# Kernel optimization log

Hardware: AMD Instinct MI355X
Metric: run time of the kernel (lower is better)

The kernel has to match this reference:

```python
import jax, jax.numpy as jnp
import numpy as np

H = 512      # hidden_size
E = 256      # encoding_size
L = 64       # latent_dim
O = 2        # output_size
NH = 4       # num_heads
HD = H // NH # head dim
BS = 1024
S = 100      # encoded source length
T = 30       # decode steps


def setup_inputs() -> dict:
    key = jax.random.key(0)
    ks = jax.random.split(key, 26)
    def p(k, shape, s=0.05):
        return jax.random.normal(k, shape, dtype=jnp.float32) * s
    return {
        "encoded": jax.random.normal(ks[0], (BS, S, E), dtype=jnp.float32),
        "z": jax.random.normal(ks[1], (BS, T, L), dtype=jnp.float32),
        # MultiheadAttention params (separate q/k/v projections since kdim!=embed_dim)
        "q_w": p(ks[2], (H, H)), "k_w": p(ks[3], (H, E)), "v_w": p(ks[4], (H, E)),
        "q_b": p(ks[5], (H,)), "k_b": p(ks[6], (H,)), "v_b": p(ks[7], (H,)),
        "out_w": p(ks[8], (H, H)), "out_b": p(ks[9], (H,)),
        # fc_layer1: Linear(H+L, H)
        "fc1_w": p(ks[10], (H, H + L)), "fc1_b": p(ks[11], (H,)),
        # LSTMCell 1 and 2 (gate order i,f,g,o)
        "l1_wih": p(ks[12], (4 * H, H)), "l1_whh": p(ks[13], (4 * H, H)),
        "l1_bih": p(ks[14], (4 * H,)), "l1_bhh": p(ks[15], (4 * H,)),
        "l2_wih": p(ks[16], (4 * H, H)), "l2_whh": p(ks[17], (4 * H, H)),
        "l2_bih": p(ks[18], (4 * H,)), "l2_bhh": p(ks[19], (4 * H,)),
        # fc_layer2: H -> H/2 -> H/4 -> O
        "fc2a_w": p(ks[20], (H // 2, H)), "fc2a_b": p(ks[21], (H // 2,)),
        "fc2b_w": p(ks[22], (H // 4, H // 2)), "fc2b_b": p(ks[23], (H // 4,)),
        "fc2c_w": p(ks[24], (O, H // 4)), "fc2c_b": p(ks[25], (O,)),
    }


def _lrelu(x):
    return jnp.where(x >= 0, x, 0.2 * x)


def _lstm_cell(x, h, c, wih, whh, bih, bhh):
    g = x @ wih.T + bih + h @ whh.T + bhh
    i, f, gg, o = jnp.split(g, 4, axis=-1)
    c2 = jax.nn.sigmoid(f) * c + jax.nn.sigmoid(i) * jnp.tanh(gg)
    h2 = jax.nn.sigmoid(o) * jnp.tanh(c2)
    return h2, c2


def _forward(encoded, z, q_w, k_w, v_w, q_b, k_b, v_b, out_w, out_b,
             fc1_w, fc1_b, l1_wih, l1_whh, l1_bih, l1_bhh,
             l2_wih, l2_whh, l2_bih, l2_bhh,
             fc2a_w, fc2a_b, fc2b_w, fc2b_b, fc2c_w, fc2c_b):
    bs, s, _ = encoded.shape
    # K/V projections depend only on encoded -> compute once: [bs, NH, S, HD]
    k = (encoded @ k_w.T + k_b).reshape(bs, s, NH, HD).transpose(0, 2, 1, 3)
    v = (encoded @ v_w.T + v_b).reshape(bs, s, NH, HD).transpose(0, 2, 1, 3)
    scale = 1.0 / jnp.sqrt(jnp.float32(HD))

    def step(carry, zt):
        att_in, h1, c1, h2, c2 = carry  # all [bs, H]
        # single-query attention (query len 1); dropout inactive in eval
        q = ((att_in @ q_w.T + q_b) * scale).reshape(bs, NH, HD)
        attw = jax.nn.softmax(jnp.einsum('bnd,bnsd->bns', q, k), axis=-1)
        att = jnp.einsum('bns,bnsd->bnd', attw, v).reshape(bs, H)
        att = att @ out_w.T + out_b
        out = _lrelu(jnp.concatenate([att, zt], axis=-1) @ fc1_w.T + fc1_b)
        h1, c1 = _lstm_cell(out, h1, c1, l1_wih, l1_whh, l1_bih, l1_bhh)
        h2, c2 = _lstm_cell(h1, h2, c2, l2_wih, l2_whh, l2_bih, l2_bhh)
        y = _lrelu(h2 @ fc2a_w.T + fc2a_b)
        y = _lrelu(y @ fc2b_w.T + fc2b_b)
        y = jnp.tanh(y @ fc2c_w.T + fc2c_b)  # [bs, O]
        return (h2, h1, c1, h2, c2), y

    zer = jnp.zeros((bs, H), dtype=encoded.dtype)
    init = (zer, zer, zer, zer, zer)
    _, ys = jax.lax.scan(step, init, jnp.swapaxes(z, 0, 1))  # ys: [T, bs, O]
    return jnp.swapaxes(ys, 0, 1)  # [bs, T, O]


def reference(encoded, z, q_w, k_w, v_w, q_b, k_b, v_b, out_w, out_b,
              fc1_w, fc1_b, l1_wih, l1_whh, l1_bih, l1_bhh,
              l2_wih, l2_whh, l2_bih, l2_bhh,
              fc2a_w, fc2a_b, fc2b_w, fc2b_b, fc2c_w, fc2c_b):
    return _forward(encoded, z, q_w, k_w, v_w, q_b, k_b, v_b, out_w, out_b,
                    fc1_w, fc1_b, l1_wih, l1_whh, l1_bih, l1_bhh,
                    l2_wih, l2_whh, l2_bih, l2_bhh,
                    fc2a_w, fc2a_b, fc2b_w, fc2b_b, fc2c_w, fc2c_b)
```

## Files before the change

kernel.cpp:

```cpp
#include <hip/hip_runtime.h>


#define DEVI __device__ __forceinline__

typedef _Float16 f16x8 __attribute__((ext_vector_type(8)));
typedef _Float16 f16x4 __attribute__((ext_vector_type(4)));
typedef float    f32x4 __attribute__((ext_vector_type(4)));
typedef unsigned u32x4 __attribute__((ext_vector_type(4)));
typedef unsigned u32x2 __attribute__((ext_vector_type(2)));

#define BSZ 1024
#define SEQ 100
#define ENC 256
#define HID 512
#define LAT 64
#define TT  30

DEVI float lrelu(float v) { return v >= 0.f ? v : 0.2f * v; }
DEVI float sigm(float x)  { return 1.f / (1.f + __expf(-x)); }
DEVI float tanh_f(float x){ return 1.f - 2.f / (1.f + __expf(2.f * x)); }

DEVI void wait_vm0() { asm volatile("s_waitcnt vmcnt(0)" ::: "memory"); }
DEVI u32x4 ld_sc_b128(const void* p) {
    u32x4 d;
    asm volatile("global_load_dwordx4 %0, %1, off sc0 sc1" : "=v"(d) : "v"(p) : "memory");
    return d;
}
DEVI void st_sc_b128(void* p, u32x4 v) {
    asm volatile("global_store_dwordx4 %0, %1, off sc0 sc1" :: "v"(p), "v"(v) : "memory");
}
DEVI void st_sc_b64(void* p, u32x2 v) {
    asm volatile("global_store_dwordx2 %0, %1, off sc0 sc1" :: "v"(p), "v"(v) : "memory");
}

__global__ __launch_bounds__(256) void zero_ws(uint4* __restrict__ p) {
    uint4 z; z.x = z.y = z.z = z.w = 0u;
    p[(size_t)blockIdx.x * 256 + threadIdx.x] = z;
}

__global__ __launch_bounds__(256) void conv_enc(const float4* __restrict__ src,
                                                f16x4* __restrict__ dst) {
    size_t i = (size_t)blockIdx.x * 256 + threadIdx.x;
    float4 v = src[i];
    f16x4 h;
    h.x = (_Float16)v.x; h.y = (_Float16)v.y; h.z = (_Float16)v.z; h.w = (_Float16)v.w;
    dst[i] = h;
}

__global__ __launch_bounds__(256) void prep_qk(const float* __restrict__ k_w,
                                               const float* __restrict__ q_w,
                                               const float* __restrict__ q_b,
                                               _Float16* __restrict__ C_h,
                                               float* __restrict__ d_f,
                                               _Float16* __restrict__ d_h) {
    const int ne = blockIdx.x, n = ne >> 8, e = ne & 255, tid = threadIdx.x;
    const float scale = 0.08838834764831845f;
    float a0 = 0.f, a1 = 0.f;
    for (int dd = 0; dd < 128; ++dd) {
        float kv = k_w[(n * 128 + dd) * 256 + e];
        a0 += kv * q_w[(n * 128 + dd) * 512 + tid];
        a1 += kv * q_w[(n * 128 + dd) * 512 + 256 + tid];
    }
    C_h[(size_t)ne * 512 + tid]       = (_Float16)(scale * a0);
    C_h[(size_t)ne * 512 + 256 + tid] = (_Float16)(scale * a1);
    float pq = (tid < 128) ? k_w[(n * 128 + tid) * 256 + e] * q_b[n * 128 + tid] : 0.f;
    #pragma unroll
    for (int off = 32; off; off >>= 1) pq += __shfl_down(pq, off);
    __shared__ float red[4];
    if ((tid & 63) == 0) red[tid >> 6] = pq;
    __syncthreads();
    if (tid == 0) {
        float s = scale * (red[0] + red[1] + red[2] + red[3]);
        d_f[ne] = s; d_h[ne] = (_Float16)s;
    }
}

__global__ __launch_bounds__(256) void prep_A(const float* __restrict__ fc1_w,
                                              const float* __restrict__ out_w,
                                              float* __restrict__ A) {
    const int h = blockIdx.x, tid = threadIdx.x;
    float a0 = 0.f, a1 = 0.f;
    for (int m = 0; m < 512; ++m) {
        float fv = fc1_w[h * 576 + m];
        a0 += fv * out_w[m * 512 + tid];
        a1 += fv * out_w[m * 512 + 256 + tid];
    }
    A[(size_t)h * 512 + tid]       = a0;
    A[(size_t)h * 512 + 256 + tid] = a1;
}

__global__ __launch_bounds__(256) void prep_wfc1(const float* __restrict__ A,
                                                 const float* __restrict__ v_w,
                                                 const float* __restrict__ v_b,
                                                 const float* __restrict__ fc1_w,
                                                 const float* __restrict__ out_b,
                                                 const float* __restrict__ fc1_b,
                                                 _Float16* __restrict__ Wfc1,
                                                 float* __restrict__ biasf) {
    const int h = blockIdx.x, tid = threadIdx.x;
    #pragma unroll
    for (int g = 0; g < 4; ++g) {
        float acc = 0.f;
        for (int dd = 0; dd < 128; ++dd)
            acc += A[h * 512 + g * 128 + dd] * v_w[(g * 128 + dd) * 256 + tid];
        Wfc1[(size_t)h * 1088 + g * 256 + tid] = (_Float16)acc;
    }
    if (tid < 64)
        Wfc1[(size_t)h * 1088 + 1024 + tid] = (_Float16)fc1_w[h * 576 + 512 + tid];
    float ps = A[h * 512 + tid] * v_b[tid] + A[h * 512 + 256 + tid] * v_b[256 + tid]
             + fc1_w[h * 576 + tid] * out_b[tid] + fc1_w[h * 576 + 256 + tid] * out_b[256 + tid];
    #pragma unroll
    for (int off = 32; off; off >>= 1) ps += __shfl_down(ps, off);
    __shared__ float red[4];
    if ((tid & 63) == 0) red[tid >> 6] = ps;
    __syncthreads();
    if (tid == 0) biasf[h] = red[0] + red[1] + red[2] + red[3] + fc1_b[h];
}

__global__ __launch_bounds__(256) void prep_lstm(const float* __restrict__ wih,
                                                 const float* __restrict__ whh,
                                                 const float* __restrict__ bih,
                                                 const float* __restrict__ bhh,
                                                 _Float16* __restrict__ Wc,
                                                 float* __restrict__ bc) {
    int idx = blockIdx.x * 256 + threadIdx.x;
    int rp = idx >> 10, cc = idx & 1023;
    int h = rp >> 2, g = rp & 3;
    int rsrc = g * 512 + h;
    float v = (cc < 512) ? wih[(size_t)rsrc * 512 + cc] : whh[(size_t)rsrc * 512 + cc - 512];
    Wc[idx] = (_Float16)v;
    if (idx < 2048) {
        int h2 = idx >> 2, g2 = idx & 3;
        bc[idx] = bih[g2 * 512 + h2] + bhh[g2 * 512 + h2];
    }
}

__global__ __launch_bounds__(256) void prep_fc2c(const float* __restrict__ aw,
                                                 const float* __restrict__ bw,
                                                 const float* __restrict__ cw,
                                                 _Float16* __restrict__ a16,
                                                 _Float16* __restrict__ b16,
                                                 _Float16* __restrict__ c16) {
    int i = blockIdx.x * 256 + threadIdx.x;
    if (i < 131072) a16[i] = (_Float16)aw[i];
    else if (i < 163840) b16[i - 131072] = (_Float16)bw[i - 131072];
    else if (i < 164096) c16[i - 163840] = (_Float16)cw[i - 163840];
}

template <int NTHR, int BM, int BN, int BK, int WM, int WN, bool BYPX>
DEVI void gemm_core_db(char* smem_raw, const _Float16* __restrict__ X, int ldx,
                       const _Float16* __restrict__ W, int ldw, int K,
                       int bm0, int bn0, f32x4* acc) {
    constexpr int LDT = BK + 8;
    _Float16* Xs = (_Float16*)smem_raw;
    _Float16* Ws = Xs + BM * LDT;
    const int tid = threadIdx.x, wave = tid >> 6, lane = tid & 63;
    constexpr int WROWS = BM / WM;
    static_assert(WROWS * (BN / WN) == NTHR / 64, "wave grid mismatch");
    const int wm = wave % WROWS, wn = wave / WROWS;
    constexpr int MT = WM / 16, NT = WN / 16;
    const int q = lane >> 4, m15 = lane & 15;
    constexpr int CPR = BK / 8;
    constexpr int XCH = BM * CPR, WCH = BN * CPR;
    constexpr int XPT = (XCH + NTHR - 1) / NTHR;
    constexpr int WPT = (WCH + NTHR - 1) / NTHR;
    u32x4 xr[XPT], wr[WPT];
    auto ldregs = [&](int k0) {
        #pragma unroll
        for (int c = 0; c < XPT; ++c) {
            int cc = tid + c * NTHR;
            if ((XCH % NTHR) == 0 || cc < XCH) {
                int row = cc / CPR, col = (cc % CPR) * 8;
                const void* px = &X[(size_t)(bm0 + row) * ldx + k0 + col];
                if (BYPX) xr[c] = ld_sc_b128(px);
                else      xr[c] = *(const u32x4*)px;
            }
        }
        #pragma unroll
        for (int c = 0; c < WPT; ++c) {
            int cc = tid + c * NTHR;
            if ((WCH % NTHR) == 0 || cc < WCH) {
                int row = cc / CPR, col = (cc % CPR) * 8;
                wr[c] = *(const u32x4*)&W[(size_t)(bn0 + row) * ldw + k0 + col];
            }
        }
    };
    ldregs(0);
    for (int k0 = 0; k0 < K; k0 += BK) {
        if (BYPX) wait_vm0();
        #pragma unroll
        for (int c = 0; c < XPT; ++c) {
            int cc = tid + c * NTHR;
            if ((XCH % NTHR) == 0 || cc < XCH) {
                int row = cc / CPR, col = (cc % CPR) * 8;
                *(u32x4*)&Xs[row * LDT + col] = xr[c];
            }
        }
        #pragma unroll
        for (int c = 0; c < WPT; ++c) {
            int cc = tid + c * NTHR;
            if ((WCH % NTHR) == 0 || cc < WCH) {
                int row = cc / CPR, col = (cc % CPR) * 8;
                *(u32x4*)&Ws[row * LDT + col] = wr[c];
            }
        }
        __syncthreads();
        if (k0 + BK < K) ldregs(k0 + BK);
        #pragma unroll
        for (int kk = 0; kk < BK / 32; ++kk) {
            f16x8 af[MT], bf[NT];
            #pragma unroll
            for (int i = 0; i < MT; ++i)
                af[i] = *(const f16x8*)&Xs[(wm * WM + i * 16 + m15) * LDT + kk * 32 + q * 8];
            #pragma unroll
            for (int j = 0; j < NT; ++j)
                bf[j] = *(const f16x8*)&Ws[(wn * WN + j * 16 + m15) * LDT + kk * 32 + q * 8];
            #pragma unroll
            for (int i = 0; i < MT; ++i)
                #pragma unroll
                for (int j = 0; j < NT; ++j)
                    acc[i * NT + j] = __builtin_amdgcn_mfma_f32_16x16x32_f16(af[i], bf[j], acc[i * NT + j], 0, 0, 0);
        }
        __syncthreads();
    }
}

template <int NTHR, int BM, int BN, int WM, int WN, int ACT>
DEVI void epi_staged(char* smem_raw, const f32x4* acc, const float* __restrict__ bias,
                     _Float16* __restrict__ out, int ldo, int bm0, int bn0) {
    constexpr int LDS_ = BN + 4;
    float* accs = (float*)smem_raw;
    const int tid = threadIdx.x, wave = tid >> 6, lane = tid & 63;
    constexpr int WROWS = BM / WM;
    const int wm = wave % WROWS, wn = wave / WROWS;
    constexpr int MT = WM / 16, NT = WN / 16;
    const int q = lane >> 4, m15 = lane & 15;
    #pragma unroll
    for (int i = 0; i < MT; ++i) {
        #pragma unroll
        for (int j = 0; j < NT; ++j) {
            int cl = wn * WN + j * 16 + m15;
            float bv = bias[bn0 + cl];
            #pragma unroll
            for (int r = 0; r < 4; ++r) {
                int rl = wm * WM + i * 16 + q * 4 + r;
                float v = acc[i * NT + j][r] + bv;
                if (ACT == 1) v = lrelu(v);
                accs[rl * LDS_ + cl] = v;
            }
        }
    }
    __syncthreads();
    constexpr int CH = BN / 8, ITEMS = BM * CH;
    #pragma unroll
    for (int base = 0; base < ITEMS; base += NTHR) {
        int idx = base + tid;
        if ((ITEMS % NTHR) == 0 || idx < ITEMS) {
            int row = idx / CH, ch = idx % CH;
            const float* src = &accs[row * LDS_ + ch * 8];
            f16x8 o;
            #pragma unroll
            for (int k = 0; k < 8; ++k) o[k] = (_Float16)src[k];
            st_sc_b128(&out[(size_t)(bm0 + row) * ldo + bn0 + ch * 8],
                       __builtin_bit_cast(u32x4, o));
        }
    }
    __syncthreads();
}

DEVI void gbar(unsigned* bars, int grp, unsigned want) {
    wait_vm0();
    __syncthreads();
    if (threadIdx.x == 0) {
        unsigned* cnt  = &bars[grp * 64];
        unsigned* flag = &bars[grp * 64 + 32];
        unsigned a = __hip_atomic_fetch_add(cnt, 1u, __ATOMIC_RELEASE, __HIP_MEMORY_SCOPE_AGENT);
        if (a == 15u) {
            __hip_atomic_store(cnt, 0u, __ATOMIC_RELAXED, __HIP_MEMORY_SCOPE_AGENT);
            __hip_atomic_store(flag, want, __ATOMIC_RELEASE, __HIP_MEMORY_SCOPE_AGENT);
        }
        unsigned spins = 0;
        while (__hip_atomic_load(flag, __ATOMIC_RELAXED, __HIP_MEMORY_SCOPE_AGENT) < want) {
            __builtin_amdgcn_s_sleep(1);
            if (++spins > (1u << 16)) break;
        }
        asm volatile("" ::: "memory");
    }
    __syncthreads();
}

DEVI void attn_phase(char* smem, const _Float16* __restrict__ G,
                     const _Float16* __restrict__ encH, const float* __restrict__ z,
                     _Float16* __restrict__ eb, int b0, int t) {
    _Float16* encs = (_Float16*)smem;
    _Float16* gs   = (_Float16*)(smem + 51200);
    float* sc      = (float*)(smem + 59392);
    float* wsm     = (float*)(smem + 61440);
    f32x4* part    = (f32x4*)(smem + 63488);
    const int tid = threadIdx.x;
    u32x4 r[7];
    auto ldenc = [&](int b) {
        const u32x4* src = (const u32x4*)(encH + (size_t)b * (SEQ * ENC));
        #pragma unroll
        for (int i = 0; i < 6; ++i) r[i] = src[tid + i * 512];
        if (tid < 128) r[6] = src[tid + 3072];
    };
    ldenc(b0);
    u32x4 gv;
    {
        int row = tid >> 7, idx = tid & 127;
        gv = ld_sc_b128(&G[(size_t)(b0 + row) * 1024 + idx * 8]);
    }
    wait_vm0();
    {
        int row = tid >> 7, idx = tid & 127;
        *(u32x4*)&gs[row * 1024 + idx * 8] = gv;
    }
    for (int i = 0; i < 4; ++i) {
        {
            u32x4* dst = (u32x4*)encs;
            #pragma unroll
            for (int k = 0; k < 6; ++k) dst[tid + k * 512] = r[k];
            if (tid < 128) dst[tid + 3072] = r[6];
        }
        __syncthreads();
        if (i < 3) ldenc(b0 + i + 1);
        const int b = b0 + i;
        {
            const int grpq = tid >> 4, l16 = tid & 15, n = grpq & 3, soff = grpq >> 2;
            const f16x8 g0 = *(const f16x8*)&gs[i * 1024 + n * 256 + l16 * 8];
            const f16x8 g1 = *(const f16x8*)&gs[i * 1024 + n * 256 + 128 + l16 * 8];
            for (int it = 0; it < 13; ++it) {
                int s = it * 8 + soff;
                if (s < SEQ) {
                    const f16x8 e0 = *(const f16x8*)&encs[s * ENC + l16 * 8];
                    const f16x8 e1 = *(const f16x8*)&encs[s * ENC + 128 + l16 * 8];
                    float p = 0.f;
                    #pragma unroll
                    for (int j = 0; j < 8; ++j)
                        p += (float)e0[j] * (float)g0[j] + (float)e1[j] * (float)g1[j];
                    p += __shfl_xor(p, 1); p += __shfl_xor(p, 2);
                    p += __shfl_xor(p, 4); p += __shfl_xor(p, 8);
                    if (l16 == 0) sc[n * 128 + s] = p;
                }
            }
        }
        __syncthreads();
        const int wv = tid >> 6, ln = tid & 63;
        if (wv < 4) {
            float v0 = sc[wv * 128 + ln];
            float v1 = (ln < SEQ - 64) ? sc[wv * 128 + 64 + ln] : -1e30f;
            float m = fmaxf(v0, v1);
            #pragma unroll
            for (int off = 32; off; off >>= 1) m = fmaxf(m, __shfl_xor(m, off));
            float e0 = __expf(v0 - m);
            float e1 = (ln < SEQ - 64) ? __expf(v1 - m) : 0.f;
            float ss = e0 + e1;
            #pragma unroll
            for (int off = 32; off; off >>= 1) ss += __shfl_xor(ss, off);
            float inv = 1.f / ss;
            wsm[wv * 128 + ln] = e0 * inv;
            if (ln < SEQ - 64) wsm[wv * 128 + 64 + ln] = e1 * inv;
        }
        __syncthreads();
        {
            const int n = wv & 3, half = wv >> 2;
            float a0 = 0.f, a1 = 0.f, a2 = 0.f, a3 = 0.f;
            const int sBeg = half * 50, sEnd = sBeg + 50;
            #pragma unroll 5
            for (int s = sBeg; s < sEnd; ++s) {
                f16x4 e4 = *(const f16x4*)&encs[s * ENC + ln * 4];
                float w = wsm[n * 128 + s];
                a0 += w * (float)e4.x; a1 += w * (float)e4.y;
                a2 += w * (float)e4.z; a3 += w * (float)e4.w;
            }
            f32x4 pv; pv[0] = a0; pv[1] = a1; pv[2] = a2; pv[3] = a3;
            part[wv * 64 + ln] = pv;
        }
        __syncthreads();
        if (tid < 128) {
            int n = tid >> 5, t8 = tid & 31;
            f32x4 a  = part[n * 64 + t8 * 2];
            f32x4 b2 = part[n * 64 + t8 * 2 + 1];
            f32x4 c  = part[(n + 4) * 64 + t8 * 2];
            f32x4 d  = part[(n + 4) * 64 + t8 * 2 + 1];
            f16x8 o;
            o[0] = (_Float16)(a[0] + c[0]); o[1] = (_Float16)(a[1] + c[1]);
            o[2] = (_Float16)(a[2] + c[2]); o[3] = (_Float16)(a[3] + c[3]);
            o[4] = (_Float16)(b2[0] + d[0]); o[5] = (_Float16)(b2[1] + d[1]);
            o[6] = (_Float16)(b2[2] + d[2]); o[7] = (_Float16)(b2[3] + d[3]);
            st_sc_b128(&eb[(size_t)b * 1088 + n * 256 + t8 * 8],
                       __builtin_bit_cast(u32x4, o));
        } else if (tid < 144) {
            int k = tid - 128;
            float4 zv = *(const float4*)&z[((size_t)b * TT + t) * 64 + k * 4];
            f16x4 zh;
            zh.x = (_Float16)zv.x; zh.y = (_Float16)zv.y;
            zh.z = (_Float16)zv.z; zh.w = (_Float16)zv.w;
            st_sc_b64(&eb[(size_t)b * 1088 + 1024 + k * 4],
                      __builtin_bit_cast(u32x2, zh));
        }
        __syncthreads();
    }
}

DEVI void lstm_phase(char* smem, const _Float16* __restrict__ X,
                     const _Float16* __restrict__ W, const float* __restrict__ bias,
                     float (&cr)[8], _Float16* __restrict__ hA, int ldA,
                     int bm0, int bn0) {
    f32x4 acc[4] = {};
    gemm_core_db<512, 64, 128, 128, 32, 32, true>(smem, X, 1024, W, 1024, 1024, bm0, bn0, acc);
    float* accs = (float*)smem;
    const int tid = threadIdx.x, wave = tid >> 6, lane = tid & 63;
    const int wm = wave & 1, wn = wave >> 1, q = lane >> 4, m15 = lane & 15;
    #pragma unroll
    for (int i = 0; i < 2; ++i) {
        #pragma unroll
        for (int j = 0; j < 2; ++j) {
            int cl = wn * 32 + j * 16 + m15;
            float bv = bias[bn0 + cl];
            #pragma unroll
            for (int r = 0; r < 4; ++r) {
                int rl = wm * 32 + i * 16 + q * 4 + r;
                accs[rl * 132 + cl] = acc[i * 2 + j][r] + bv;
            }
        }
    }
    __syncthreads();
    if (tid < 256) {
        int bl = tid >> 2, ch = tid & 3;
        const float4* gp = (const float4*)&accs[bl * 132 + ch * 32];
        f16x8 hv;
        #pragma unroll
        for (int j = 0; j < 8; ++j) {
            float4 g4 = gp[j];
            float cn = sigm(g4.y) * cr[j] + sigm(g4.x) * tanh_f(g4.z);
            cr[j] = cn;
            hv[j] = (_Float16)(sigm(g4.w) * tanh_f(cn));
        }
        int h0 = (bn0 >> 2) + ch * 8, gb = bm0 + bl;
        st_sc_b128(&hA[(size_t)gb * ldA + h0], __builtin_bit_cast(u32x4, hv));
    }
    __syncthreads();
}

DEVI void fc2_512(char* smem, const _Float16* __restrict__ h2n,
                  const _Float16* __restrict__ Wa, const float* __restrict__ ab,
                  const _Float16* __restrict__ Wb, const float* __restrict__ bb,
                  const _Float16* __restrict__ Wc, const float* __restrict__ cb,
                  float* __restrict__ out, int b0, int t) {
    _Float16* h2s = (_Float16*)smem;
    _Float16* y1s = h2s + 16 * 520;
    _Float16* y2s = y1s + 16 * 264;
    const int tid = threadIdx.x, wave = tid >> 6, lane = tid & 63;
    const int q = lane >> 4, m15 = lane & 15;
    u32x4 hv[2];
    #pragma unroll
    for (int c = 0; c < 2; ++c) {
        int cc = tid + c * 512, row = cc >> 6, col = (cc & 63) * 8;
        hv[c] = ld_sc_b128(&h2n[(size_t)(b0 + row) * 512 + col]);
    }
    wait_vm0();
    #pragma unroll
    for (int c = 0; c < 2; ++c) {
        int cc = tid + c * 512, row = cc >> 6, col = (cc & 63) * 8;
        *(u32x4*)&h2s[row * 520 + col] = hv[c];
    }
    __syncthreads();
    {
        f32x4 acc[2] = {};
        #pragma unroll 4
        for (int kk = 0; kk < 16; ++kk) {
            f16x8 af = *(const f16x8*)&h2s[m15 * 520 + kk * 32 + q * 8];
            #pragma unroll
            for (int j = 0; j < 2; ++j) {
                int n = wave * 32 + j * 16 + m15;
                f16x8 bf = *(const f16x8*)&Wa[(size_t)n * 512 + kk * 32 + q * 8];
                acc[j] = __builtin_amdgcn_mfma_f32_16x16x32_f16(af, bf, acc[j], 0, 0, 0);
            }
        }
        #pragma unroll
        for (int j = 0; j < 2; ++j) {
            int col = wave * 32 + j * 16 + m15;
            float bv = ab[col];
            #pragma unroll
            for (int r = 0; r < 4; ++r)
                y1s[(q * 4 + r) * 264 + col] = (_Float16)lrelu(acc[j][r] + bv);
        }
    }
    __syncthreads();
    {
        f32x4 acc[1] = {};
        #pragma unroll
        for (int kk = 0; kk < 8; ++kk) {
            f16x8 af = *(const f16x8*)&y1s[m15 * 264 + kk * 32 + q * 8];
            int n = wave * 16 + m15;
            f16x8 bf = *(const f16x8*)&Wb[(size_t)n * 256 + kk * 32 + q * 8];
            acc[0] = __builtin_amdgcn_mfma_f32_16x16x32_f16(af, bf, acc[0], 0, 0, 0);
        }
        int col = wave * 16 + m15;
        float bv = bb[col];
        #pragma unroll
        for (int r = 0; r < 4; ++r)
            y2s[(q * 4 + r) * 136 + col] = (_Float16)lrelu(acc[0][r] + bv);
    }
    __syncthreads();
    if (tid < 32) {
        int r = tid >> 1, o = tid & 1;
        float acc = cb[o];
        #pragma unroll 8
        for (int k = 0; k < 128; ++k)
            acc += (float)Wc[o * 128 + k] * (float)y2s[r * 136 + k];
        out[((size_t)(b0 + r) * TT + t) * 2 + o] = tanhf(acc);
    }
}

struct DecP {
    const _Float16* encH;
    const float* z;
    _Float16* eb;
    const _Float16* Wfc1;  const float* biasf;
    const _Float16* L1W;   const float* L1b;
    const _Float16* L2W;   const float* L2b;
    const _Float16* C_h;   const float* d_f;  const _Float16* d_h;
    const _Float16* fa;    const float* fab;
    const _Float16* fb;    const float* fbb;
    const _Float16* fcw;   const float* fcb;
    _Float16* xh1;  _Float16* xh2;  _Float16* h2n;  _Float16* G;
    float* out;
    unsigned* bars;
};

__global__ __launch_bounds__(512, 1) void decoder(DecP p) {
    __shared__ __align__(16) char smem[71680];
    const int blk = blockIdx.x, tid = threadIdx.x;
    const int grp = blk >> 4, sub = blk & 15;
    const int b0a = blk * 4;
    const int bm0 = grp * 64;
    float c1r[8] = {}, c2r[8] = {};
    unsigned want = 0;
    if (tid < 128) {
        u32x4 v = *(const u32x4*)&p.d_h[tid * 8];
        #pragma unroll
        for (int i = 0; i < 4; ++i)
            st_sc_b128(&p.G[(size_t)(b0a + i) * 1024 + tid * 8], v);
    }
    wait_vm0();
    __syncthreads();
    for (int t = 0; t < TT; ++t) {
        attn_phase(smem, p.G, p.encH, p.z, p.eb, b0a, t);
        gbar(p.bars, grp, ++want);
        {
            f32x4 acc[1] = {};
            gemm_core_db<512, 64, 32, 64, 16, 16, true>(smem, p.eb, 1088, p.Wfc1, 1088, 1088,
                                                        bm0, sub * 32, acc);
            epi_staged<512, 64, 32, 16, 16, 1>(smem, acc, p.biasf, p.xh1, 1024, bm0, sub * 32);
        }
        gbar(p.bars, grp, ++want);
        lstm_phase(smem, p.xh1, p.L1W, p.L1b, c1r, p.xh2, 1024, bm0, sub * 128);
        gbar(p.bars, grp, ++want);
        lstm_phase(smem, p.xh2, p.L2W, p.L2b, c2r, p.h2n, 512, bm0, sub * 128);
        gbar(p.bars, grp, ++want);
        if (t < TT - 1) {
            {
                int idx = tid & 255, row = idx >> 2, ch = idx & 3;
                size_t ro = (size_t)(bm0 + row);
                const void* src; void* dst;
                if (tid < 256) {
                    src = &p.xh2[ro * 1024 + sub * 32 + ch * 8];
                    dst = &p.xh1[ro * 1024 + 512 + sub * 32 + ch * 8];
                } else {
                    src = &p.h2n[ro * 512 + sub * 32 + ch * 8];
                    dst = &p.xh2[ro * 1024 + 512 + sub * 32 + ch * 8];
                }
                u32x4 v = ld_sc_b128(src);
                wait_vm0();
                st_sc_b128(dst, v);
            }
            f32x4 acc[2] = {};
            gemm_core_db<512, 64, 64, 128, 16, 32, true>(smem, p.h2n, 512, p.C_h, 512, 512,
                                                         bm0, sub * 64, acc);
            epi_staged<512, 64, 64, 16, 32, 0>(smem, acc, p.d_f, p.G, 1024, bm0, sub * 64);
        }
        if (sub < 4)
            fc2_512(smem, p.h2n, p.fa, p.fab, p.fb, p.fbb, p.fcw, p.fcb,
                    p.out, bm0 + sub * 16, t);
        if (t < TT - 1) gbar(p.bars, grp, ++want);
    }
}

extern "C" void kernel_launch(void* const* d_in, const int* in_sizes, int n_in,
                              void* d_out, int out_size, void* d_ws, size_t ws_size,
                              hipStream_t stream) {
    const float* encoded = (const float*)d_in[0];
    const float* z       = (const float*)d_in[1];
    const float* q_w     = (const float*)d_in[2];
    const float* k_w     = (const float*)d_in[3];
    const float* v_w     = (const float*)d_in[4];
    const float* q_b     = (const float*)d_in[5];
    const float* v_b     = (const float*)d_in[7];
    const float* out_w   = (const float*)d_in[8];
    const float* out_b   = (const float*)d_in[9];
    const float* fc1_w   = (const float*)d_in[10];
    const float* fc1_b   = (const float*)d_in[11];
    const float* l1_wih  = (const float*)d_in[12];
    const float* l1_whh  = (const float*)d_in[13];
    const float* l1_bih  = (const float*)d_in[14];
    const float* l1_bhh  = (const float*)d_in[15];
    const float* l2_wih  = (const float*)d_in[16];
    const float* l2_whh  = (const float*)d_in[17];
    const float* l2_bih  = (const float*)d_in[18];
    const float* l2_bhh  = (const float*)d_in[19];
    const float* fc2a_w  = (const float*)d_in[20];
    const float* fc2a_b  = (const float*)d_in[21];
    const float* fc2b_w  = (const float*)d_in[22];
    const float* fc2b_b  = (const float*)d_in[23];
    const float* fc2c_w  = (const float*)d_in[24];
    const float* fc2c_b  = (const float*)d_in[25];
    float* out = (float*)d_out;

    char* p = (char*)d_ws;
    auto take = [&](size_t bytes) { char* r = p; p += (bytes + 255) & ~(size_t)255; return r; };
    _Float16* encH  = (_Float16*)take(52428800);
    _Float16* C_h   = (_Float16*)take(1048576);
    _Float16* Wfc1  = (_Float16*)take(1114112);
    _Float16* L1W   = (_Float16*)take(4194304);
    _Float16* L2W   = (_Float16*)take(4194304);
    _Float16* fc2a16= (_Float16*)take(262144);
    _Float16* fc2b16= (_Float16*)take(65536);
    _Float16* fc2c16= (_Float16*)take(512);
    _Float16* eb    = (_Float16*)take(2228224);
    _Float16* h2n   = (_Float16*)take(1048576);
    char* zreg = p;
    _Float16* xh1 = (_Float16*)take(2097152);
    _Float16* xh2 = (_Float16*)take(2097152);
    unsigned* bars = (unsigned*)take(4096);
    _Float16* G   = (_Float16*)take(2097152);
    float* A      = (float*)take(1048576);
    float* d_f    = (float*)take(4096);
    _Float16* d_h = (_Float16*)take(2048);
    float* biasf  = (float*)take(2048);
    float* L1b    = (float*)take(8192);
    float* L2b    = (float*)take(8192);
    (void)in_sizes; (void)n_in; (void)out_size; (void)ws_size;

    zero_ws<<<1025, 256, 0, stream>>>((uint4*)zreg);
    conv_enc<<<25600, 256, 0, stream>>>((const float4*)encoded, (f16x4*)encH);
    prep_qk<<<1024, 256, 0, stream>>>(k_w, q_w, q_b, C_h, d_f, d_h);
    prep_A<<<512, 256, 0, stream>>>(fc1_w, out_w, A);
    prep_wfc1<<<512, 256, 0, stream>>>(A, v_w, v_b, fc1_w, out_b, fc1_b, Wfc1, biasf);
    prep_lstm<<<8192, 256, 0, stream>>>(l1_wih, l1_whh, l1_bih, l1_bhh, L1W, L1b);
    prep_lstm<<<8192, 256, 0, stream>>>(l2_wih, l2_whh, l2_bih, l2_bhh, L2W, L2b);
    prep_fc2c<<<641, 256, 0, stream>>>(fc2a_w, fc2b_w, fc2c_w, fc2a16, fc2b16, fc2c16);

    DecP dp;
    dp.encH = encH; dp.z = z; dp.eb = eb;
    dp.Wfc1 = Wfc1; dp.biasf = biasf;
    dp.L1W = L1W; dp.L1b = L1b; dp.L2W = L2W; dp.L2b = L2b;
    dp.C_h = C_h; dp.d_f = d_f; dp.d_h = d_h;
    dp.fa = fc2a16; dp.fab = fc2a_b; dp.fb = fc2b16; dp.fbb = fc2b_b;
    dp.fcw = fc2c16; dp.fcb = fc2c_b;
    dp.xh1 = xh1; dp.xh2 = xh2; dp.h2n = h2n; dp.G = G;
    dp.out = out; dp.bars = bars;
    void* params[] = { &dp };
    if (hipLaunchCooperativeKernel((const void*)decoder, dim3(256), dim3(512),
                                   params, 0, stream) != hipSuccess) {
        decoder<<<256, 512, 0, stream>>>(dp);
    }
}
```

Baseline: 3.309 ms.

## Keep encoder slices resident in LDS/registers, double-buffer hidden state, flag-array barrier

Each block now loads its four encoder slices once before the decode loop, one into shared memory and three into registers, instead of re-reading them from global memory on every step. The recurrent hidden-state buffers are double-buffered, and the LSTM epilogue writes h into the next step's input buffer directly, which removes the copy phase. The group barrier swaps the atomic counter for per-block flag stores that every block polls with vector loads. The cost is a much larger register footprint (84 extra u32x4 per thread) and more shared memory. Launch bounds also change to 2 blocks per CU, which could spill or hurt occupancy.

```diff
diff --git a/kernel.cpp b/kernel.cpp
--- a/kernel.cpp
+++ b/kernel.cpp
@@ -19,6 +19,7 @@
 DEVI float lrelu(float v) { return v >= 0.f ? v : 0.2f * v; }
 DEVI float sigm(float x)  { return 1.f / (1.f + __expf(-x)); }
 DEVI float tanh_f(float x){ return 1.f - 2.f / (1.f + __expf(2.f * x)); }
+DEVI unsigned umin2(unsigned a, unsigned b) { return a < b ? a : b; }
 
 DEVI void wait_vm0() { asm volatile("s_waitcnt vmcnt(0)" ::: "memory"); }
 DEVI u32x4 ld_sc_b128(const void* p) {
@@ -31,6 +32,9 @@
 }
 DEVI void st_sc_b64(void* p, u32x2 v) {
     asm volatile("global_store_dwordx2 %0, %1, off sc0 sc1" :: "v"(p), "v"(v) : "memory");
+}
+DEVI void st_sc_b32(void* p, unsigned v) {
+    asm volatile("global_store_dword %0, %1, off sc0 sc1" :: "v"(p), "v"(v) : "memory");
 }
 
 __global__ __launch_bounds__(256) void zero_ws(uint4* __restrict__ p) {
@@ -268,146 +272,148 @@
     __syncthreads();
 }
 
-DEVI void gbar(unsigned* bars, int grp, unsigned want) {
+DEVI void gbar(unsigned* bars, int grp, int sub, unsigned want) {
     wait_vm0();
     __syncthreads();
     if (threadIdx.x == 0) {
-        unsigned* cnt  = &bars[grp * 64];
-        unsigned* flag = &bars[grp * 64 + 32];
-        unsigned a = __hip_atomic_fetch_add(cnt, 1u, __ATOMIC_RELEASE, __HIP_MEMORY_SCOPE_AGENT);
-        if (a == 15u) {
-            __hip_atomic_store(cnt, 0u, __ATOMIC_RELAXED, __HIP_MEMORY_SCOPE_AGENT);
-            __hip_atomic_store(flag, want, __ATOMIC_RELEASE, __HIP_MEMORY_SCOPE_AGENT);
-        }
+        st_sc_b32(&bars[grp * 16 + sub], want);
         unsigned spins = 0;
-        while (__hip_atomic_load(flag, __ATOMIC_RELAXED, __HIP_MEMORY_SCOPE_AGENT) < want) {
+        for (;;) {
+            u32x4 a = ld_sc_b128(&bars[grp * 16 + 0]);
+            u32x4 b = ld_sc_b128(&bars[grp * 16 + 4]);
+            u32x4 c = ld_sc_b128(&bars[grp * 16 + 8]);
+            u32x4 d = ld_sc_b128(&bars[grp * 16 + 12]);
+            wait_vm0();
+            unsigned mn = umin2(umin2(umin2(a[0], a[1]), umin2(a[2], a[3])),
+                          umin2(umin2(umin2(b[0], b[1]), umin2(b[2], b[3])),
+                          umin2(umin2(umin2(c[0], c[1]), umin2(c[2], c[3])),
+                                umin2(umin2(d[0], d[1]), umin2(d[2], d[3])))));
+            if (mn >= want) break;
             __builtin_amdgcn_s_sleep(1);
-            if (++spins > (1u << 16)) break;
+            if (++spins > (1u << 17)) break;
         }
         asm volatile("" ::: "memory");
     }
     __syncthreads();
 }
 
-DEVI void attn_phase(char* smem, const _Float16* __restrict__ G,
-                     const _Float16* __restrict__ encH, const float* __restrict__ z,
+DEVI void attn_one(const _Float16* encs, const _Float16* gs, float* sc, float* wsm,
+                   f32x4* part, const float* __restrict__ z,
+                   _Float16* __restrict__ eb, int gi, int b, int t) {
+    const int tid = threadIdx.x;
+    {
+        const int grpq = tid >> 4, l16 = tid & 15, n = grpq & 3, soff = grpq >> 2;
+        const f16x8 g0 = *(const f16x8*)&gs[gi * 1024 + n * 256 + l16 * 8];
+        const f16x8 g1 = *(const f16x8*)&gs[gi * 1024 + n * 256 + 128 + l16 * 8];
+        for (int it = 0; it < 13; ++it) {
+            int s = it * 8 + soff;
+            if (s < SEQ) {
+                const f16x8 e0 = *(const f16x8*)&encs[s * ENC + l16 * 8];
+                const f16x8 e1 = *(const f16x8*)&encs[s * ENC + 128 + l16 * 8];
+                float p = 0.f;
+                #pragma unroll
+                for (int j = 0; j < 8; ++j)
+                    p += (float)e0[j] * (float)g0[j] + (float)e1[j] * (float)g1[j];
+                p += __shfl_xor(p, 1); p += __shfl_xor(p, 2);
+                p += __shfl_xor(p, 4); p += __shfl_xor(p, 8);
+                if (l16 == 0) sc[n * 128 + s] = p;
+            }
+        }
+    }
+    __syncthreads();
+    const int wv = tid >> 6, ln = tid & 63;
+    if (wv < 4) {
+        float v0 = sc[wv * 128 + ln];
+        float v1 = (ln < SEQ - 64) ? sc[wv * 128 + 64 + ln] : -1e30f;
+        float m = fmaxf(v0, v1);
+        #pragma unroll
+        for (int off = 32; off; off >>= 1) m = fmaxf(m, __shfl_xor(m, off));
+        float e0 = __expf(v0 - m);
+        float e1 = (ln < SEQ - 64) ? __expf(v1 - m) : 0.f;
+        float ss = e0 + e1;
+        #pragma unroll
+        for (int off = 32; off; off >>= 1) ss += __shfl_xor(ss, off);
+        float inv = 1.f / ss;
+        wsm[wv * 128 + ln] = e0 * inv;
+        if (ln < SEQ - 64) wsm[wv * 128 + 64 + ln] = e1 * inv;
+    }
+    __syncthreads();
+    {
+        const int n = wv & 3, half = wv >> 2;
+        float a0 = 0.f, a1 = 0.f, a2 = 0.f, a3 = 0.f;
+        const int sBeg = half * 50, sEnd = sBeg + 50;
+        #pragma unroll 5
+        for (int s = sBeg; s < sEnd; ++s) {
+            f16x4 e4 = *(const f16x4*)&encs[s * ENC + ln * 4];
+            float w = wsm[n * 128 + s];
+            a0 += w * (float)e4.x; a1 += w * (float)e4.y;
+            a2 += w * (float)e4.z; a3 += w * (float)e4.w;
+        }
+        f32x4 pv; pv[0] = a0; pv[1] = a1; pv[2] = a2; pv[3] = a3;
+        part[wv * 64 + ln] = pv;
+    }
+    __syncthreads();
+    if (tid < 128) {
+        int n = tid >> 5, t8 = tid & 31;
+        f32x4 a  = part[n * 64 + t8 * 2];
+        f32x4 b2 = part[n * 64 + t8 * 2 + 1];
+        f32x4 c  = part[(n + 4) * 64 + t8 * 2];
+        f32x4 d  = part[(n + 4) * 64 + t8 * 2 + 1];
+        f16x8 o;
+        o[0] = (_Float16)(a[0] + c[0]); o[1] = (_Float16)(a[1] + c[1]);
+        o[2] = (_Float16)(a[2] + c[2]); o[3] = (_Float16)(a[3] + c[3]);
+        o[4] = (_Float16)(b2[0] + d[0]); o[5] = (_Float16)(b2[1] + d[1]);
+        o[6] = (_Float16)(b2[2] + d[2]); o[7] = (_Float16)(b2[3] + d[3]);
+        st_sc_b128(&eb[(size_t)b * 1088 + n * 256 + t8 * 8],
+                   __builtin_bit_cast(u32x4, o));
+    } else if (tid < 144) {
+        int k = tid - 128;
+        float4 zv = *(const float4*)&z[((size_t)b * TT + t) * 64 + k * 4];
+        f16x4 zh;
+        zh.x = (_Float16)zv.x; zh.y = (_Float16)zv.y;
+        zh.z = (_Float16)zv.z; zh.w = (_Float16)zv.w;
+        st_sc_b64(&eb[(size_t)b * 1088 + 1024 + k * 4],
+                  __builtin_bit_cast(u32x2, zh));
+    }
+    __syncthreads();
+}
+
+DEVI void attn_phase(char* smem_all, u32x4 (&er)[3][7],
+                     const _Float16* __restrict__ G, const float* __restrict__ z,
                      _Float16* __restrict__ eb, int b0, int t) {
-    _Float16* encs = (_Float16*)smem;
-    _Float16* gs   = (_Float16*)(smem + 51200);
-    float* sc      = (float*)(smem + 59392);
-    float* wsm     = (float*)(smem + 61440);
-    f32x4* part    = (f32x4*)(smem + 63488);
+    _Float16* encP  = (_Float16*)smem_all;
+    char* scratch   = smem_all + 51200;
+    _Float16* stage = (_Float16*)scratch;
+    _Float16* gs    = (_Float16*)(scratch + 51200);
+    float* sc       = (float*)(scratch + 59392);
+    float* wsm      = (float*)(scratch + 61440);
+    f32x4* part     = (f32x4*)(scratch + 63488);
     const int tid = threadIdx.x;
-    u32x4 r[7];
-    auto ldenc = [&](int b) {
-        const u32x4* src = (const u32x4*)(encH + (size_t)b * (SEQ * ENC));
-        #pragma unroll
-        for (int i = 0; i < 6; ++i) r[i] = src[tid + i * 512];
-        if (tid < 128) r[6] = src[tid + 3072];
-    };
-    ldenc(b0);
-    u32x4 gv;
     {
         int row = tid >> 7, idx = tid & 127;
-        gv = ld_sc_b128(&G[(size_t)(b0 + row) * 1024 + idx * 8]);
-    }
-    wait_vm0();
-    {
-        int row = tid >> 7, idx = tid & 127;
+        u32x4 gv = ld_sc_b128(&G[(size_t)(b0 + row) * 1024 + idx * 8]);
+        wait_vm0();
         *(u32x4*)&gs[row * 1024 + idx * 8] = gv;
     }
-    for (int i = 0; i < 4; ++i) {
+    __syncthreads();
+    attn_one(encP, gs, sc, wsm, part, z, eb, 0, b0, t);
+    #pragma unroll
+    for (int i = 0; i < 3; ++i) {
         {
-            u32x4* dst = (u32x4*)encs;
-            #pragma unroll
-            for (int k = 0; k < 6; ++k) dst[tid + k * 512] = r[k];
-            if (tid < 128) dst[tid + 3072] = r[6];
+            u32x4* dst = (u32x4*)stage;
+            #pragma unroll
+            for (int k = 0; k < 6; ++k) dst[tid + k * 512] = er[i][k];
+            if (tid < 128) dst[tid + 3072] = er[i][6];
         }
         __syncthreads();
-        if (i < 3) ldenc(b0 + i + 1);
-        const int b = b0 + i;
-        {
-            const int grpq = tid >> 4, l16 = tid & 15, n = grpq & 3, soff = grpq >> 2;
-            const f16x8 g0 = *(const f16x8*)&gs[i * 1024 + n * 256 + l16 * 8];
-            const f16x8 g1 = *(const f16x8*)&gs[i * 1024 + n * 256 + 128 + l16 * 8];
-            for (int it = 0; it < 13; ++it) {
-                int s = it * 8 + soff;
-                if (s < SEQ) {
-                    const f16x8 e0 = *(const f16x8*)&encs[s * ENC + l16 * 8];
-                    const f16x8 e1 = *(const f16x8*)&encs[s * ENC + 128 + l16 * 8];
-                    float p = 0.f;
-                    #pragma unroll
-                    for (int j = 0; j < 8; ++j)
-                        p += (float)e0[j] * (float)g0[j] + (float)e1[j] * (float)g1[j];
-                    p += __shfl_xor(p, 1); p += __shfl_xor(p, 2);
-                    p += __shfl_xor(p, 4); p += __shfl_xor(p, 8);
-                    if (l16 == 0) sc[n * 128 + s] = p;
-                }
-            }
-        }
-        __syncthreads();
-        const int wv = tid >> 6, ln = tid & 63;
-        if (wv < 4) {
-            float v0 = sc[wv * 128 + ln];
-            float v1 = (ln < SEQ - 64) ? sc[wv * 128 + 64 + ln] : -1e30f;
-            float m = fmaxf(v0, v1);
-            #pragma unroll
-            for (int off = 32; off; off >>= 1) m = fmaxf(m, __shfl_xor(m, off));
-            float e0 = __expf(v0 - m);
-            float e1 = (ln < SEQ - 64) ? __expf(v1 - m) : 0.f;
-            float ss = e0 + e1;
-            #pragma unroll
-            for (int off = 32; off; off >>= 1) ss += __shfl_xor(ss, off);
-            float inv = 1.f / ss;
-            wsm[wv * 128 + ln] = e0 * inv;
-            if (ln < SEQ - 64) wsm[wv * 128 + 64 + ln] = e1 * inv;
-        }
-        __syncthreads();
-        {
-            const int n = wv & 3, half = wv >> 2;
-            float a0 = 0.f, a1 = 0.f, a2 = 0.f, a3 = 0.f;
-            const int sBeg = half * 50, sEnd = sBeg + 50;
-            #pragma unroll 5
-            for (int s = sBeg; s < sEnd; ++s) {
-                f16x4 e4 = *(const f16x4*)&encs[s * ENC + ln * 4];
-                float w = wsm[n * 128 + s];
-                a0 += w * (float)e4.x; a1 += w * (float)e4.y;
-                a2 += w * (float)e4.z; a3 += w * (float)e4.w;
-            }
-            f32x4 pv; pv[0] = a0; pv[1] = a1; pv[2] = a2; pv[3] = a3;
-            part[wv * 64 + ln] = pv;
-        }
-        __syncthreads();
-        if (tid < 128) {
-            int n = tid >> 5, t8 = tid & 31;
-            f32x4 a  = part[n * 64 + t8 * 2];
-            f32x4 b2 = part[n * 64 + t8 * 2 + 1];
-            f32x4 c  = part[(n + 4) * 64 + t8 * 2];
-            f32x4 d  = part[(n + 4) * 64 + t8 * 2 + 1];
-            f16x8 o;
-            o[0] = (_Float16)(a[0] + c[0]); o[1] = (_Float16)(a[1] + c[1]);
-            o[2] = (_Float16)(a[2] + c[2]); o[3] = (_Float16)(a[3] + c[3]);
-            o[4] = (_Float16)(b2[0] + d[0]); o[5] = (_Float16)(b2[1] + d[1]);
-            o[6] = (_Float16)(b2[2] + d[2]); o[7] = (_Float16)(b2[3] + d[3]);
-            st_sc_b128(&eb[(size_t)b * 1088 + n * 256 + t8 * 8],
-                       __builtin_bit_cast(u32x4, o));
-        } else if (tid < 144) {
-            int k = tid - 128;
-            float4 zv = *(const float4*)&z[((size_t)b * TT + t) * 64 + k * 4];
-            f16x4 zh;
-            zh.x = (_Float16)zv.x; zh.y = (_Float16)zv.y;
-            zh.z = (_Float16)zv.z; zh.w = (_Float16)zv.w;
-            st_sc_b64(&eb[(size_t)b * 1088 + 1024 + k * 4],
-                      __builtin_bit_cast(u32x2, zh));
-        }
-        __syncthreads();
+        attn_one(stage, gs, sc, wsm, part, z, eb, i + 1, b0 + 1 + i, t);
     }
 }
 
 DEVI void lstm_phase(char* smem, const _Float16* __restrict__ X,
                      const _Float16* __restrict__ W, const float* __restrict__ bias,
                      float (&cr)[8], _Float16* __restrict__ hA, int ldA,
-                     int bm0, int bn0) {
+                     _Float16* __restrict__ hB, int ldB, int bm0, int bn0) {
     f32x4 acc[4] = {};
     gemm_core_db<512, 64, 128, 128, 32, 32, true>(smem, X, 1024, W, 1024, 1024, bm0, bn0, acc);
     float* accs = (float*)smem;
@@ -439,7 +445,9 @@
             hv[j] = (_Float16)(sigm(g4.w) * tanh_f(cn));
         }
         int h0 = (bn0 >> 2) + ch * 8, gb = bm0 + bl;
-        st_sc_b128(&hA[(size_t)gb * ldA + h0], __builtin_bit_cast(u32x4, hv));
+        u32x4 hb = __builtin_bit_cast(u32x4, hv);
+        st_sc_b128(&hA[(size_t)gb * ldA + h0], hb);
+        st_sc_b128(&hB[(size_t)gb * ldB + h0], hb);
     }
     __syncthreads();
 }
@@ -526,19 +534,35 @@
     const _Float16* fa;    const float* fab;
     const _Float16* fb;    const float* fbb;
     const _Float16* fcw;   const float* fcb;
-    _Float16* xh1;  _Float16* xh2;  _Float16* h2n;  _Float16* G;
+    _Float16* xh1[2];  _Float16* xh2[2];  _Float16* h2n;  _Float16* G;
     float* out;
     unsigned* bars;
 };
 
-__global__ __launch_bounds__(512, 1) void decoder(DecP p) {
-    __shared__ __align__(16) char smem[71680];
+__global__ __launch_bounds__(512, 2) void decoder(DecP p) {
+    __shared__ __align__(16) char smem[122880];
+    char* scratch = smem + 51200;
     const int blk = blockIdx.x, tid = threadIdx.x;
     const int grp = blk >> 4, sub = blk & 15;
     const int b0a = blk * 4;
     const int bm0 = grp * 64;
     float c1r[8] = {}, c2r[8] = {};
+    u32x4 er[3][7];
     unsigned want = 0;
+    {
+        const u32x4* s0 = (const u32x4*)(p.encH + (size_t)b0a * (SEQ * ENC));
+        u32x4* encP = (u32x4*)smem;
+        #pragma unroll
+        for (int k = 0; k < 6; ++k) encP[tid + k * 512] = s0[tid + k * 512];
+        if (tid < 128) encP[tid + 3072] = s0[tid + 3072];
+        #pragma unroll
+        for (int i = 0; i < 3; ++i) {
+            const u32x4* si = (const u32x4*)(p.encH + (size_t)(b0a + 1 + i) * (SEQ * ENC));
+            #pragma unroll
+            for (int k = 0; k < 6; ++k) er[i][k] = si[tid + k * 512];
+            if (tid < 128) er[i][6] = si[tid + 3072];
+        }
+    }
     if (tid < 128) {
         u32x4 v = *(const u32x4*)&p.d_h[tid * 8];
         #pragma unroll
@@ -548,44 +572,32 @@
     wait_vm0();
     __syncthreads();
     for (int t = 0; t < TT; ++t) {
-        attn_phase(smem, p.G, p.encH, p.z, p.eb, b0a, t);
-        gbar(p.bars, grp, ++want);
+        const int pt = t & 1;
+        attn_phase(smem, er, p.G, p.z, p.eb, b0a, t);
+        gbar(p.bars, grp, sub, ++want);
         {
             f32x4 acc[1] = {};
-            gemm_core_db<512, 64, 32, 64, 16, 16, true>(smem, p.eb, 1088, p.Wfc1, 1088, 1088,
+            gemm_core_db<512, 64, 32, 64, 16, 16, true>(scratch, p.eb, 1088, p.Wfc1, 1088, 1088,
                                                         bm0, sub * 32, acc);
-            epi_staged<512, 64, 32, 16, 16, 1>(smem, acc, p.biasf, p.xh1, 1024, bm0, sub * 32);
-        }
-        gbar(p.bars, grp, ++want);
-        lstm_phase(smem, p.xh1, p.L1W, p.L1b, c1r, p.xh2, 1024, bm0, sub * 128);
-        gbar(p.bars, grp, ++want);
-        lstm_phase(smem, p.xh2, p.L2W, p.L2b, c2r, p.h2n, 512, bm0, sub * 128);
-        gbar(p.bars, grp, ++want);
+            epi_staged<512, 64, 32, 16, 16, 1>(scratch, acc, p.biasf, p.xh1[pt], 1024, bm0, sub * 32);
+        }
+        gbar(p.bars, grp, sub, ++want);
+        lstm_phase(scratch, p.xh1[pt], p.L1W, p.L1b, c1r,
+                   p.xh2[pt], 1024, p.xh1[pt ^ 1] + 512, 1024, bm0, sub * 128);
+        gbar(p.bars, grp, sub, ++want);
+        lstm_phase(scratch, p.xh2[pt], p.L2W, p.L2b, c2r,
+                   p.h2n, 512, p.xh2[pt ^ 1] + 512, 1024, bm0, sub * 128);
+        gbar(p.bars, grp, sub, ++want);
         if (t < TT - 1) {
-            {
-                int idx = tid & 255, row = idx >> 2, ch = idx & 3;
-                size_t ro = (size_t)(bm0 + row);
-                const void* src; void* dst;
-                if (tid < 256) {
-                    src = &p.xh2[ro * 1024 + sub * 32 + ch * 8];
-                    dst = &p.xh1[ro * 1024 + 512 + sub * 32 + ch * 8];
-                } else {
-                    src = &p.h2n[ro * 512 + sub * 32 + ch * 8];
-                    dst = &p.xh2[ro * 1024 + 512 + sub * 32 + ch * 8];
-                }
-                u32x4 v = ld_sc_b128(src);
-                wait_vm0();
-                st_sc_b128(dst, v);
-            }
             f32x4 acc[2] = {};
-            gemm_core_db<512, 64, 64, 128, 16, 32, true>(smem, p.h2n, 512, p.C_h, 512, 512,
+            gemm_core_db<512, 64, 64, 128, 16, 32, true>(scratch, p.h2n, 512, p.C_h, 512, 512,
                                                          bm0, sub * 64, acc);
-            epi_staged<512, 64, 64, 16, 32, 0>(smem, acc, p.d_f, p.G, 1024, bm0, sub * 64);
+            epi_staged<512, 64, 64, 16, 32, 0>(scratch, acc, p.d_f, p.G, 1024, bm0, sub * 64);
         }
         if (sub < 4)
-            fc2_512(smem, p.h2n, p.fa, p.fab, p.fb, p.fbb, p.fcw, p.fcb,
+            fc2_512(scratch, p.h2n, p.fa, p.fab, p.fb, p.fbb, p.fcw, p.fcb,
                     p.out, bm0 + sub * 16, t);
-        if (t < TT - 1) gbar(p.bars, grp, ++want);
+        if (t < TT - 1) gbar(p.bars, grp, sub, ++want);
     }
 }
 
@@ -632,8 +644,10 @@
     _Float16* eb    = (_Float16*)take(2228224);
     _Float16* h2n   = (_Float16*)take(1048576);
     char* zreg = p;
-    _Float16* xh1 = (_Float16*)take(2097152);
-    _Float16* xh2 = (_Float16*)take(2097152);
+    _Float16* xh1a = (_Float16*)take(2097152);
+    _Float16* xh1b = (_Float16*)take(2097152);
+    _Float16* xh2a = (_Float16*)take(2097152);
+    _Float16* xh2b = (_Float16*)take(2097152);
     unsigned* bars = (unsigned*)take(4096);
     _Float16* G   = (_Float16*)take(2097152);
     float* A      = (float*)take(1048576);
@@ -644,7 +658,7 @@
     float* L2b    = (float*)take(8192);
     (void)in_sizes; (void)n_in; (void)out_size; (void)ws_size;
 
-    zero_ws<<<1025, 256, 0, stream>>>((uint4*)zreg);
+    zero_ws<<<2049, 256, 0, stream>>>((uint4*)zreg);
     conv_enc<<<25600, 256, 0, stream>>>((const float4*)encoded, (f16x4*)encH);
     prep_qk<<<1024, 256, 0, stream>>>(k_w, q_w, q_b, C_h, d_f, d_h);
     prep_A<<<512, 256, 0, stream>>>(fc1_w, out_w, A);
@@ -660,7 +674,9 @@
     dp.C_h = C_h; dp.d_f = d_f; dp.d_h = d_h;
     dp.fa = fc2a16; dp.fab = fc2a_b; dp.fb = fc2b16; dp.fbb = fc2b_b;
     dp.fcw = fc2c16; dp.fcb = fc2c_b;
-    dp.xh1 = xh1; dp.xh2 = xh2; dp.h2n = h2n; dp.G = G;
+    dp.xh1[0] = xh1a; dp.xh1[1] = xh1b;
+    dp.xh2[0] = xh2a; dp.xh2[1] = xh2b;
+    dp.h2n = h2n; dp.G = G;
     dp.out = out; dp.bars = bars;
     void* params[] = { &dp };
     if (hipLaunchCooperativeKernel((const void*)decoder, dim3(256), dim3(512),
```

New measurement: 3.132 ms. -5.4%, faster.
